# Optimization experiments

Hardware: AMD Instinct MI355X
Metric: run time of the kernel (lower is better)

Reference implementation:

```python
import math
import jax, jax.numpy as jnp
import numpy as np

GROUPS = 32
EPS = 1e-5


def group_norm(x, w, b):
    # x: [B, C, H, W]
    B, C, H, W = x.shape
    xg = x.reshape(B, GROUPS, C // GROUPS, H, W)
    mean = xg.mean(axis=(2, 3, 4), keepdims=True)
    var = xg.var(axis=(2, 3, 4), keepdims=True)
    xg = (xg - mean) * jax.lax.rsqrt(var + EPS)
    x = xg.reshape(B, C, H, W)
    return x * w[None, :, None, None] + b[None, :, None, None]


def setup_inputs() -> dict:
    key = jax.random.key(0)
    ks = jax.random.split(key, 4)
    B, C, H, W = 16, 512, 32, 32
    x = jax.random.normal(ks[0], (B, C, H, W), dtype=jnp.float32)
    norm_w = jnp.ones((C,), dtype=jnp.float32)
    norm_b = jnp.zeros((C,), dtype=jnp.float32)
    qkv_w = jax.random.normal(ks[1], (3 * C, C), dtype=jnp.float32) / math.sqrt(C)
    qkv_b = jnp.zeros((3 * C,), dtype=jnp.float32)
    proj_w = jax.random.normal(ks[2], (C, C), dtype=jnp.float32) / math.sqrt(C)
    proj_b = jnp.zeros((C,), dtype=jnp.float32)
    return {"x": x, "norm_w": norm_w, "norm_b": norm_b,
            "qkv_w": qkv_w, "qkv_b": qkv_b,
            "proj_w": proj_w, "proj_b": proj_b}


def reference(x, norm_w, norm_b, qkv_w, qkv_b, proj_w, proj_b):
    B, C, H, W = x.shape
    xn = group_norm(x, norm_w, norm_b)
    # 1x1 conv == channel matmul: [B,3C,H,W]
    qkv = jnp.einsum('oc,bchw->bohw', qkv_w, xn) + qkv_b[None, :, None, None]
    q, k, v = jnp.split(qkv, 3, axis=1)
    q = q.reshape(B, C, H * W).transpose(0, 2, 1)  # [B, HW, C]
    k = k.reshape(B, C, H * W)                     # [B, C, HW]
    v = v.reshape(B, C, H * W).transpose(0, 2, 1)  # [B, HW, C]
    attn = jax.nn.softmax(jnp.einsum('bnc,bcm->bnm', q, k) / math.sqrt(C), axis=-1)
    h = jnp.einsum('bnm,bmc->bnc', attn, v)        # [B, HW, C]
    h = h.transpose(0, 2, 1).reshape(B, C, H, W)
    out = jnp.einsum('oc,bchw->bohw', proj_w, h) + proj_b[None, :, None, None]
    return out + x
```

## Files before the change

### kernel.cpp

```cpp
#include <hip/hip_runtime.h>

#define GLD16(gp, lp) __builtin_amdgcn_global_load_lds( \
    (const __attribute__((address_space(1))) void*)(gp), \
    (__attribute__((address_space(3))) void*)(lp), 16, 0, 0)

typedef __attribute__((ext_vector_type(8))) short bf16x8;
typedef __attribute__((ext_vector_type(4))) float f32x4;

__device__ __forceinline__ short f2bf(float f) {
    union { float f; unsigned u; } x; x.f = f;
    unsigned r = x.u + 0x7fffu + ((x.u >> 16) & 1u);
    return (short)(r >> 16);
}
__device__ __forceinline__ float bf2f(short s) {
    union { unsigned u; float f; } x;
    x.u = ((unsigned)(unsigned short)s) << 16;
    return x.f;
}
__device__ __forceinline__ int xcd_swz(int id, int n) {
    return (id & 7) * (n >> 3) + (id >> 3);
}

__global__ __launch_bounds__(256) void prep(
    const float* __restrict__ qkv_w, const float* __restrict__ proj_w,
    short* __restrict__ wq, short* __restrict__ wp,
    const float* __restrict__ x, float* __restrict__ mean, float* __restrict__ rstd)
{
    if (blockIdx.x < 1024) {
        int idx = blockIdx.x * 256 + threadIdx.x;
        const int NQ4 = (1536 * 512) / 4;
        float4 f; short4 s;
        if (idx < NQ4) {
            f = ((const float4*)qkv_w)[idx];
            s.x = f2bf(f.x); s.y = f2bf(f.y); s.z = f2bf(f.z); s.w = f2bf(f.w);
            ((short4*)wq)[idx] = s;
        } else {
            int j = idx - NQ4;
            f = ((const float4*)proj_w)[j];
            s.x = f2bf(f.x); s.y = f2bf(f.y); s.z = f2bf(f.z); s.w = f2bf(f.w);
            ((short4*)wp)[j] = s;
        }
    } else {
        int bg = blockIdx.x - 1024;
        const float4* p = (const float4*)(x + (size_t)bg * 16384);
        float s = 0.f, ss = 0.f;
        for (int i = threadIdx.x; i < 4096; i += 256) {
            float4 v = p[i];
            s  += v.x + v.y + v.z + v.w;
            ss += v.x * v.x + v.y * v.y + v.z * v.z + v.w * v.w;
        }
        #pragma unroll
        for (int o = 32; o > 0; o >>= 1) {
            s  += __shfl_down(s, o);
            ss += __shfl_down(ss, o);
        }
        __shared__ float ls[4], lss[4];
        int wave = threadIdx.x >> 6;
        if ((threadIdx.x & 63) == 0) { ls[wave] = s; lss[wave] = ss; }
        __syncthreads();
        if (threadIdx.x == 0) {
            s  = ls[0] + ls[1] + ls[2] + ls[3];
            ss = lss[0] + lss[1] + lss[2] + lss[3];
            float m = s * (1.f / 16384.f);
            float var = ss * (1.f / 16384.f) - m * m;
            mean[bg] = m;
            rstd[bg] = rsqrtf(var + 1e-5f);
        }
    }
}

__global__ __launch_bounds__(256) void gn_apply_t(
    const float* __restrict__ x, const float* __restrict__ w, const float* __restrict__ bb,
    const float* __restrict__ mean, const float* __restrict__ rstd,
    short* __restrict__ xnT)
{
    __shared__ short tile[64][65];
    int b = blockIdx.z, cblk = blockIdx.y, nblk = blockIdx.x;
    int t = threadIdx.x;
    int nl = t & 63;
    int cb = t >> 6;
    #pragma unroll
    for (int i = 0; i < 16; ++i) {
        int cl = cb * 16 + i;
        int cg = cblk * 64 + cl;
        int bgid = b * 32 + (cg >> 4);
        float sc = rstd[bgid] * w[cg];
        float sh = bb[cg] - mean[bgid] * sc;
        float xv = x[((size_t)(b * 512 + cg)) * 1024 + nblk * 64 + nl];
        tile[cl][nl] = f2bf(xv * sc + sh);
    }
    __syncthreads();
    int ng = t >> 4;
    int c4 = (t & 15) * 4;
    #pragma unroll
    for (int p = 0; p < 4; ++p) {
        int nl2 = p * 16 + ng;
        short4 sv;
        sv.x = tile[c4 + 0][nl2];
        sv.y = tile[c4 + 1][nl2];
        sv.z = tile[c4 + 2][nl2];
        sv.w = tile[c4 + 3][nl2];
        *(short4*)&xnT[((size_t)(b * 1024 + nblk * 64 + nl2)) * 512 + cblk * 64 + c4] = sv;
    }
}

template<int NT>
__device__ __forceinline__ void gemm256_8p(
    const short* __restrict__ A, const short* __restrict__ B,
    const int lda, const int ldb, short* lds, f32x4 acc[8][4])
{
    const int tid  = threadIdx.x;
    const int lane = tid & 63;
    const int wave = tid >> 6;
    const int wm = wave >> 2;
    const int wn = wave & 3;
    const int fr = lane & 15;
    const int fk = lane >> 4;

    const short* pa[2]; const short* pb[2]; int la[2], lb[2];
    #pragma unroll
    for (int i = 0; i < 2; ++i) {
        int cid = i * 512 + tid;
        int row = cid >> 2, sl = cid & 3;
        int csw = sl ^ ((row >> 1) & 3);
        pa[i] = A + (size_t)row * lda + csw * 8;
        pb[i] = B + (size_t)row * ldb + csw * 8;
        la[i] = cid * 8;
        lb[i] = 8192 + cid * 8;
    }

    #pragma unroll
    for (int i = 0; i < 2; ++i) GLD16(pa[i],      lds + la[i]);
    #pragma unroll
    for (int i = 0; i < 2; ++i) GLD16(pb[i],      lds + lb[i]);
    #pragma unroll
    for (int i = 0; i < 2; ++i) GLD16(pa[i] + 32, lds + 16384 + la[i]);
    #pragma unroll
    for (int i = 0; i < 2; ++i) GLD16(pb[i] + 32, lds + 16384 + lb[i]);
    asm volatile("s_waitcnt vmcnt(4)" ::: "memory");
    asm volatile("s_barrier" ::: "memory");

    const int arow0 = wm * 128 + fr;
    const int brow0 = wn * 64 + fr;

    int base = 0, sbase = 32768, kst = 64;
    for (int t = 0; t < NT; ++t) {
        const short* lA = lds + base;
        const short* lB = lds + base + 8192;
        const bool pre = (t + 2 < NT);

        if (pre) {
            GLD16(pa[0] + kst, lds + sbase + la[0]);
            GLD16(pa[1] + kst, lds + sbase + la[1]);
        }
        bf16x8 af[8], bf0[2];
        #pragma unroll
        for (int m = 0; m < 8; ++m) {
            int R = arow0 + m * 16;
            af[m] = *(const bf16x8*)&lA[R * 32 + ((fk ^ ((R >> 1) & 3)) << 3)];
        }
        #pragma unroll
        for (int n = 0; n < 2; ++n) {
            int R = brow0 + n * 16;
            bf0[n] = *(const bf16x8*)&lB[R * 32 + ((fk ^ ((R >> 1) & 3)) << 3)];
        }
        asm volatile("s_barrier" ::: "memory");
        __builtin_amdgcn_s_setprio(1);
        #pragma unroll
        for (int m = 0; m < 8; ++m)
            #pragma unroll
            for (int n = 0; n < 2; ++n)
                acc[m][n] = __builtin_amdgcn_mfma_f32_16x16x32_bf16(af[m], bf0[n], acc[m][n], 0, 0, 0);
        __builtin_amdgcn_s_setprio(0);

        if (pre) {
            GLD16(pb[0] + kst, lds + sbase + lb[0]);
            GLD16(pb[1] + kst, lds + sbase + lb[1]);
        }
        bf16x8 bf1[2];
        #pragma unroll
        for (int n = 0; n < 2; ++n) {
            int R = brow0 + (n + 2) * 16;
            bf1[n] = *(const bf16x8*)&lB[R * 32 + ((fk ^ ((R >> 1) & 3)) << 3)];
        }
        asm volatile("s_barrier" ::: "memory");
        __builtin_amdgcn_s_setprio(1);
        #pragma unroll
        for (int m = 0; m < 8; ++m)
            #pragma unroll
            for (int n = 0; n < 2; ++n)
                acc[m][n + 2] = __builtin_amdgcn_mfma_f32_16x16x32_bf16(af[m], bf1[n], acc[m][n + 2], 0, 0, 0);
        __builtin_amdgcn_s_setprio(0);

        if (pre)                 asm volatile("s_waitcnt vmcnt(4)" ::: "memory");
        else if (t + 1 < NT)     asm volatile("s_waitcnt vmcnt(0)" ::: "memory");
        asm volatile("s_barrier" ::: "memory");
        __builtin_amdgcn_sched_barrier(0);
        base  = (base  == 32768) ? 0 : base  + 16384;
        sbase = (sbase == 32768) ? 0 : sbase + 16384;
        kst += 32;
    }
}

#define EPI_IDX() \
    const int lane = threadIdx.x & 63; \
    const int wave = threadIdx.x >> 6; \
    const int wm = wave >> 2; \
    const int wn = wave & 3; \
    const int fq = lane >> 4; \
    const int fcol = lane & 15;

__global__ __launch_bounds__(512, 2) void qkv_gemm(
    const short* __restrict__ wq, const float* __restrict__ qkv_b,
    const short* __restrict__ xnT,
    short* __restrict__ qT, short* __restrict__ kT, short* __restrict__ vv)
{
    __shared__ short lds[49152];
    int wg = xcd_swz(blockIdx.x, 384);
    const int bn = wg & 3, bm = (wg >> 2) % 6, b = wg / 24;
    const short* A  = wq + (size_t)bm * 256 * 512;
    const short* Bb = xnT + ((size_t)b * 1024 + bn * 256) * 512;
    f32x4 acc[8][4];
    #pragma unroll
    for (int m = 0; m < 8; ++m)
        #pragma unroll
        for (int n = 0; n < 4; ++n) acc[m][n] = (f32x4){0.f, 0.f, 0.f, 0.f};
    gemm256_8p<16>(A, Bb, 512, 512, lds, acc);

    EPI_IDX();
    const int region = bm >> 1;
    const float qscale = 0.04419417382415922f;

    #pragma unroll
    for (int m = 0; m < 8; ++m) {
        int o0 = bm * 256 + wm * 128 + m * 16 + fq * 4;
        float4 bias = *(const float4*)&qkv_b[o0];
        float bb4[4] = {bias.x, bias.y, bias.z, bias.w};
        #pragma unroll
        for (int n = 0; n < 4; ++n) {
            int col = bn * 256 + wn * 64 + n * 16 + fcol;
            f32x4 a = acc[m][n];
            if (region == 0) {
                short4 sv;
                sv.x = f2bf((a[0] + bb4[0]) * qscale);
                sv.y = f2bf((a[1] + bb4[1]) * qscale);
                sv.z = f2bf((a[2] + bb4[2]) * qscale);
                sv.w = f2bf((a[3] + bb4[3]) * qscale);
                *(short4*)&qT[((size_t)(b * 1024 + col)) * 512 + o0] = sv;
            } else if (region == 1) {
                short4 sv;
                sv.x = f2bf(a[0] + bb4[0]);
                sv.y = f2bf(a[1] + bb4[1]);
                sv.z = f2bf(a[2] + bb4[2]);
                sv.w = f2bf(a[3] + bb4[3]);
                *(short4*)&kT[((size_t)(b * 1024 + col)) * 512 + (o0 - 512)] = sv;
            } else {
                #pragma unroll
                for (int r = 0; r < 4; ++r)
                    vv[((size_t)(b * 512 + (o0 - 1024 + r))) * 1024 + col] = f2bf(a[r] + bb4[r]);
            }
        }
    }
}

__global__ __launch_bounds__(512, 2) void s_gemm(
    const short* __restrict__ kT, const short* __restrict__ qT, short* __restrict__ S)
{
    __shared__ short lds[49152];
    int wg = xcd_swz(blockIdx.x, 256);
    const int bn = wg & 3, bm = (wg >> 2) & 3, b = wg >> 4;
    const short* A  = kT + ((size_t)b * 1024 + bm * 256) * 512;
    const short* Bb = qT + ((size_t)b * 1024 + bn * 256) * 512;
    f32x4 acc[8][4];
    #pragma unroll
    for (int m = 0; m < 8; ++m)
        #pragma unroll
        for (int n = 0; n < 4; ++n) acc[m][n] = (f32x4){0.f, 0.f, 0.f, 0.f};
    gemm256_8p<16>(A, Bb, 512, 512, lds, acc);

    EPI_IDX();
    #pragma unroll
    for (int m = 0; m < 8; ++m) {
        int m0 = bm * 256 + wm * 128 + m * 16 + fq * 4;
        #pragma unroll
        for (int n = 0; n < 4; ++n) {
            int ncol = bn * 256 + wn * 64 + n * 16 + fcol;
            f32x4 a = acc[m][n];
            short4 sv;
            sv.x = f2bf(a[0]); sv.y = f2bf(a[1]); sv.z = f2bf(a[2]); sv.w = f2bf(a[3]);
            *(short4*)&S[((size_t)(b * 1024 + ncol)) * 1024 + m0] = sv;
        }
    }
}

__global__ __launch_bounds__(256) void softmax_rows(short* __restrict__ S)
{
    const int wave = threadIdx.x >> 6;
    const int lane = threadIdx.x & 63;
    size_t row = (size_t)blockIdx.x * 4 + wave;
    short* p = S + row * 1024;
    short4 raw[4];
    float v[16];
    #pragma unroll
    for (int i = 0; i < 4; ++i) raw[i] = ((short4*)p)[lane + 64 * i];
    #pragma unroll
    for (int i = 0; i < 4; ++i) {
        v[i * 4 + 0] = bf2f(raw[i].x);
        v[i * 4 + 1] = bf2f(raw[i].y);
        v[i * 4 + 2] = bf2f(raw[i].z);
        v[i * 4 + 3] = bf2f(raw[i].w);
    }
    float mx = v[0];
    #pragma unroll
    for (int i = 1; i < 16; ++i) mx = fmaxf(mx, v[i]);
    #pragma unroll
    for (int o = 1; o < 64; o <<= 1) mx = fmaxf(mx, __shfl_xor(mx, o));
    float sum = 0.f;
    #pragma unroll
    for (int i = 0; i < 16; ++i) { v[i] = __expf(v[i] - mx); sum += v[i]; }
    #pragma unroll
    for (int o = 1; o < 64; o <<= 1) sum += __shfl_xor(sum, o);
    float inv = 1.f / sum;
    #pragma unroll
    for (int i = 0; i < 4; ++i) {
        short4 sv;
        sv.x = f2bf(v[i * 4 + 0] * inv);
        sv.y = f2bf(v[i * 4 + 1] * inv);
        sv.z = f2bf(v[i * 4 + 2] * inv);
        sv.w = f2bf(v[i * 4 + 3] * inv);
        ((short4*)p)[lane + 64 * i] = sv;
    }
}

__global__ __launch_bounds__(512, 2) void pv_gemm(
    const short* __restrict__ vv, const short* __restrict__ P, short* __restrict__ h)
{
    __shared__ short lds[49152];
    int wg = xcd_swz(blockIdx.x, 128);
    const int bn = wg & 3, bm = (wg >> 2) & 1, b = wg >> 3;
    const short* A  = vv + ((size_t)b * 512 + bm * 256) * 1024;
    const short* Bb = P + ((size_t)b * 1024 + bn * 256) * 1024;
    f32x4 acc[8][4];
    #pragma unroll
    for (int m = 0; m < 8; ++m)
        #pragma unroll
        for (int n = 0; n < 4; ++n) acc[m][n] = (f32x4){0.f, 0.f, 0.f, 0.f};
    gemm256_8p<32>(A, Bb, 1024, 1024, lds, acc);

    EPI_IDX();
    #pragma unroll
    for (int m = 0; m < 8; ++m) {
        int c0 = bm * 256 + wm * 128 + m * 16 + fq * 4;
        #pragma unroll
        for (int n = 0; n < 4; ++n) {
            int ncol = bn * 256 + wn * 64 + n * 16 + fcol;
            f32x4 a = acc[m][n];
            short4 sv;
            sv.x = f2bf(a[0]); sv.y = f2bf(a[1]); sv.z = f2bf(a[2]); sv.w = f2bf(a[3]);
            *(short4*)&h[((size_t)(b * 1024 + ncol)) * 512 + c0] = sv;
        }
    }
}

__global__ __launch_bounds__(512, 2) void proj_gemm(
    const short* __restrict__ wp, const float* __restrict__ proj_b,
    const short* __restrict__ h, const float* __restrict__ x, float* __restrict__ out)
{
    __shared__ short lds[49152];
    int wg = xcd_swz(blockIdx.x, 128);
    const int bn = wg & 3, bm = (wg >> 2) & 1, b = wg >> 3;
    const short* A  = wp + (size_t)bm * 256 * 512;
    const short* Bb = h + ((size_t)b * 1024 + bn * 256) * 512;
    f32x4 acc[8][4];
    #pragma unroll
    for (int m = 0; m < 8; ++m)
        #pragma unroll
        for (int n = 0; n < 4; ++n) acc[m][n] = (f32x4){0.f, 0.f, 0.f, 0.f};
    gemm256_8p<16>(A, Bb, 512, 512, lds, acc);

    EPI_IDX();
    #pragma unroll
    for (int m = 0; m < 8; ++m) {
        int o0 = bm * 256 + wm * 128 + m * 16 + fq * 4;
        float4 pb = *(const float4*)&proj_b[o0];
        float pb4[4] = {pb.x, pb.y, pb.z, pb.w};
        #pragma unroll
        for (int n = 0; n < 4; ++n) {
            int col = bn * 256 + wn * 64 + n * 16 + fcol;
            f32x4 a = acc[m][n];
            #pragma unroll
            for (int r = 0; r < 4; ++r) {
                size_t idx = ((size_t)(b * 512 + o0 + r)) * 1024 + col;
                out[idx] = a[r] + pb4[r] + x[idx];
            }
        }
    }
}

extern "C" void kernel_launch(void* const* d_in, const int* in_sizes, int n_in,
                              void* d_out, int out_size, void* d_ws, size_t ws_size,
                              hipStream_t stream) {
    const float* x      = (const float*)d_in[0];
    const float* norm_w = (const float*)d_in[1];
    const float* norm_b = (const float*)d_in[2];
    const float* qkv_w  = (const float*)d_in[3];
    const float* qkv_b  = (const float*)d_in[4];
    const float* proj_w = (const float*)d_in[5];
    const float* proj_b = (const float*)d_in[6];
    float* out = (float*)d_out;

    char* ws = (char*)d_ws;
    size_t off = 0;
    auto alloc = [&](size_t bytes) {
        void* p = ws + off;
        off = (off + bytes + 255) & ~(size_t)255;
        return p;
    };
    float* mean = (float*)alloc(512 * 4);
    float* rstd = (float*)alloc(512 * 4);
    short* wq   = (short*)alloc((size_t)1536 * 512 * 2);
    short* wp   = (short*)alloc((size_t)512 * 512 * 2);
    short* xnT  = (short*)alloc((size_t)16 * 1024 * 512 * 2);
    short* qT   = (short*)alloc((size_t)16 * 1024 * 512 * 2);
    short* kT   = (short*)alloc((size_t)16 * 1024 * 512 * 2);
    short* vv   = (short*)alloc((size_t)16 * 512 * 1024 * 2);
    short* S    = (short*)alloc((size_t)16 * 1024 * 1024 * 2);
    short* h    = xnT;

    prep<<<1536, 256, 0, stream>>>(qkv_w, proj_w, wq, wp, x, mean, rstd);
    gn_apply_t<<<dim3(16, 8, 16), 256, 0, stream>>>(x, norm_w, norm_b, mean, rstd, xnT);
    qkv_gemm<<<384, 512, 0, stream>>>(wq, qkv_b, xnT, qT, kT, vv);
    s_gemm<<<256, 512, 0, stream>>>(kT, qT, S);
    softmax_rows<<<4096, 256, 0, stream>>>(S);
    pv_gemm<<<128, 512, 0, stream>>>(vv, S, h);
    proj_gemm<<<128, 512, 0, stream>>>(wp, proj_b, h, x, out);
}
```

Measured before the change: 243.1 us.

## Use 128x256 GEMM tiles for PV and projection to double workgroup count

Adds a 128x256 tile GEMM variant with a smaller 3-stage LDS footprint and uses it for pv_gemm and proj_gemm, so each launches 256 workgroups instead of 128. The goal is to fill more of the 256 CUs, which were underused by the two smaller GEMMs. It also remaps the qkv and proj tile indices to treat batch and spatial as one flattened N dimension. Smaller tiles lower per-block data reuse and raise global traffic for the A operand.

```diff
diff --git a/kernel.cpp b/kernel.cpp
--- a/kernel.cpp
+++ b/kernel.cpp
@@ -202,7 +202,105 @@
     }
 }
 
-#define EPI_IDX() \
+template<int NT>
+__device__ __forceinline__ void gemm128x256(
+    const short* __restrict__ A, const short* __restrict__ B,
+    const int lda, const int ldb, short* lds, f32x4 acc[4][4])
+{
+    const int tid  = threadIdx.x;
+    const int lane = tid & 63;
+    const int wave = tid >> 6;
+    const int wm = wave >> 2;
+    const int wn = wave & 3;
+    const int fr = lane & 15;
+    const int fk = lane >> 4;
+
+    const short* pa; int la;
+    {
+        int row = tid >> 2, sl = tid & 3;
+        int csw = sl ^ ((row >> 1) & 3);
+        pa = A + (size_t)row * lda + csw * 8;
+        la = tid * 8;
+    }
+    const short* pb[2]; int lb[2];
+    #pragma unroll
+    for (int i = 0; i < 2; ++i) {
+        int cid = i * 512 + tid;
+        int row = cid >> 2, sl = cid & 3;
+        int csw = sl ^ ((row >> 1) & 3);
+        pb[i] = B + (size_t)row * ldb + csw * 8;
+        lb[i] = 4096 + cid * 8;
+    }
+
+    GLD16(pa, lds + la);
+    #pragma unroll
+    for (int i = 0; i < 2; ++i) GLD16(pb[i], lds + lb[i]);
+    GLD16(pa + 32, lds + 12288 + la);
+    #pragma unroll
+    for (int i = 0; i < 2; ++i) GLD16(pb[i] + 32, lds + 12288 + lb[i]);
+    asm volatile("s_waitcnt vmcnt(3)" ::: "memory");
+    asm volatile("s_barrier" ::: "memory");
+
+    const int arow0 = wm * 64 + fr;
+    const int brow0 = wn * 64 + fr;
+
+    int base = 0, sbase = 24576, kst = 64;
+    for (int t = 0; t < NT; ++t) {
+        const short* lA = lds + base;
+        const short* lB = lds + base + 4096;
+        const bool pre = (t + 2 < NT);
+
+        if (pre) GLD16(pa + kst, lds + sbase + la);
+        bf16x8 af[4], bf0[2];
+        #pragma unroll
+        for (int m = 0; m < 4; ++m) {
+            int R = arow0 + m * 16;
+            af[m] = *(const bf16x8*)&lA[R * 32 + ((fk ^ ((R >> 1) & 3)) << 3)];
+        }
+        #pragma unroll
+        for (int n = 0; n < 2; ++n) {
+            int R = brow0 + n * 16;
+            bf0[n] = *(const bf16x8*)&lB[R * 32 + ((fk ^ ((R >> 1) & 3)) << 3)];
+        }
+        asm volatile("s_barrier" ::: "memory");
+        __builtin_amdgcn_s_setprio(1);
+        #pragma unroll
+        for (int m = 0; m < 4; ++m)
+            #pragma unroll
+            for (int n = 0; n < 2; ++n)
+                acc[m][n] = __builtin_amdgcn_mfma_f32_16x16x32_bf16(af[m], bf0[n], acc[m][n], 0, 0, 0);
+        __builtin_amdgcn_s_setprio(0);
+
+        if (pre) {
+            GLD16(pb[0] + kst, lds + sbase + lb[0]);
+            GLD16(pb[1] + kst, lds + sbase + lb[1]);
+        }
+        bf16x8 bf1[2];
+        #pragma unroll
+        for (int n = 0; n < 2; ++n) {
+            int R = brow0 + (n + 2) * 16;
+            bf1[n] = *(const bf16x8*)&lB[R * 32 + ((fk ^ ((R >> 1) & 3)) << 3)];
+        }
+        asm volatile("s_barrier" ::: "memory");
+        __builtin_amdgcn_s_setprio(1);
+        #pragma unroll
+        for (int m = 0; m < 4; ++m)
+            #pragma unroll
+            for (int n = 0; n < 2; ++n)
+                acc[m][n + 2] = __builtin_amdgcn_mfma_f32_16x16x32_bf16(af[m], bf1[n], acc[m][n + 2], 0, 0, 0);
+        __builtin_amdgcn_s_setprio(0);
+
+        if (pre)                 asm volatile("s_waitcnt vmcnt(3)" ::: "memory");
+        else if (t + 1 < NT)     asm volatile("s_waitcnt vmcnt(0)" ::: "memory");
+        asm volatile("s_barrier" ::: "memory");
+        __builtin_amdgcn_sched_barrier(0);
+        base  = (base  == 24576) ? 0 : base  + 12288;
+        sbase = (sbase == 24576) ? 0 : sbase + 12288;
+        kst += 32;
+    }
+}
+
+#define EPI_IDX8() \
     const int lane = threadIdx.x & 63; \
     const int wave = threadIdx.x >> 6; \
     const int wm = wave >> 2; \
@@ -217,9 +315,9 @@
 {
     __shared__ short lds[49152];
     int wg = xcd_swz(blockIdx.x, 384);
-    const int bn = wg & 3, bm = (wg >> 2) % 6, b = wg / 24;
+    const int bm = wg % 6, bn = wg / 6;
     const short* A  = wq + (size_t)bm * 256 * 512;
-    const short* Bb = xnT + ((size_t)b * 1024 + bn * 256) * 512;
+    const short* Bb = xnT + (size_t)bn * 256 * 512;
     f32x4 acc[8][4];
     #pragma unroll
     for (int m = 0; m < 8; ++m)
@@ -227,7 +325,7 @@
         for (int n = 0; n < 4; ++n) acc[m][n] = (f32x4){0.f, 0.f, 0.f, 0.f};
     gemm256_8p<16>(A, Bb, 512, 512, lds, acc);
 
-    EPI_IDX();
+    EPI_IDX8();
     const int region = bm >> 1;
     const float qscale = 0.04419417382415922f;
 
@@ -238,7 +336,8 @@
         float bb4[4] = {bias.x, bias.y, bias.z, bias.w};
         #pragma unroll
         for (int n = 0; n < 4; ++n) {
-            int col = bn * 256 + wn * 64 + n * 16 + fcol;
+            int cf = bn * 256 + wn * 64 + n * 16 + fcol;
+            int b = cf >> 10, col = cf & 1023;
             f32x4 a = acc[m][n];
             if (region == 0) {
                 short4 sv;
@@ -278,7 +377,7 @@
         for (int n = 0; n < 4; ++n) acc[m][n] = (f32x4){0.f, 0.f, 0.f, 0.f};
     gemm256_8p<16>(A, Bb, 512, 512, lds, acc);
 
-    EPI_IDX();
+    EPI_IDX8();
     #pragma unroll
     for (int m = 0; m < 8; ++m) {
         int m0 = bm * 256 + wm * 128 + m * 16 + fq * 4;
@@ -332,25 +431,25 @@
     }
 }
 
-__global__ __launch_bounds__(512, 2) void pv_gemm(
+__global__ __launch_bounds__(512, 4) void pv_gemm(
     const short* __restrict__ vv, const short* __restrict__ P, short* __restrict__ h)
 {
-    __shared__ short lds[49152];
-    int wg = xcd_swz(blockIdx.x, 128);
-    const int bn = wg & 3, bm = (wg >> 2) & 1, b = wg >> 3;
-    const short* A  = vv + ((size_t)b * 512 + bm * 256) * 1024;
+    __shared__ short lds[36864];
+    int wg = xcd_swz(blockIdx.x, 256);
+    const int bn = wg & 3, bm = (wg >> 2) & 3, b = wg >> 4;
+    const short* A  = vv + ((size_t)b * 512 + bm * 128) * 1024;
     const short* Bb = P + ((size_t)b * 1024 + bn * 256) * 1024;
-    f32x4 acc[8][4];
-    #pragma unroll
-    for (int m = 0; m < 8; ++m)
+    f32x4 acc[4][4];
+    #pragma unroll
+    for (int m = 0; m < 4; ++m)
         #pragma unroll
         for (int n = 0; n < 4; ++n) acc[m][n] = (f32x4){0.f, 0.f, 0.f, 0.f};
-    gemm256_8p<32>(A, Bb, 1024, 1024, lds, acc);
-
-    EPI_IDX();
-    #pragma unroll
-    for (int m = 0; m < 8; ++m) {
-        int c0 = bm * 256 + wm * 128 + m * 16 + fq * 4;
+    gemm128x256<32>(A, Bb, 1024, 1024, lds, acc);
+
+    EPI_IDX8();
+    #pragma unroll
+    for (int m = 0; m < 4; ++m) {
+        int c0 = bm * 128 + wm * 64 + m * 16 + fq * 4;
         #pragma unroll
         for (int n = 0; n < 4; ++n) {
             int ncol = bn * 256 + wn * 64 + n * 16 + fcol;
@@ -362,31 +461,32 @@
     }
 }
 
-__global__ __launch_bounds__(512, 2) void proj_gemm(
+__global__ __launch_bounds__(512, 4) void proj_gemm(
     const short* __restrict__ wp, const float* __restrict__ proj_b,
     const short* __restrict__ h, const float* __restrict__ x, float* __restrict__ out)
 {
-    __shared__ short lds[49152];
-    int wg = xcd_swz(blockIdx.x, 128);
-    const int bn = wg & 3, bm = (wg >> 2) & 1, b = wg >> 3;
-    const short* A  = wp + (size_t)bm * 256 * 512;
-    const short* Bb = h + ((size_t)b * 1024 + bn * 256) * 512;
-    f32x4 acc[8][4];
-    #pragma unroll
-    for (int m = 0; m < 8; ++m)
+    __shared__ short lds[36864];
+    int wg = xcd_swz(blockIdx.x, 256);
+    const int bm = wg & 3, bn = wg >> 2;
+    const short* A  = wp + (size_t)bm * 128 * 512;
+    const short* Bb = h + (size_t)bn * 256 * 512;
+    f32x4 acc[4][4];
+    #pragma unroll
+    for (int m = 0; m < 4; ++m)
         #pragma unroll
         for (int n = 0; n < 4; ++n) acc[m][n] = (f32x4){0.f, 0.f, 0.f, 0.f};
-    gemm256_8p<16>(A, Bb, 512, 512, lds, acc);
-
-    EPI_IDX();
-    #pragma unroll
-    for (int m = 0; m < 8; ++m) {
-        int o0 = bm * 256 + wm * 128 + m * 16 + fq * 4;
+    gemm128x256<16>(A, Bb, 512, 512, lds, acc);
+
+    EPI_IDX8();
+    #pragma unroll
+    for (int m = 0; m < 4; ++m) {
+        int o0 = bm * 128 + wm * 64 + m * 16 + fq * 4;
         float4 pb = *(const float4*)&proj_b[o0];
         float pb4[4] = {pb.x, pb.y, pb.z, pb.w};
         #pragma unroll
         for (int n = 0; n < 4; ++n) {
-            int col = bn * 256 + wn * 64 + n * 16 + fcol;
+            int cf = bn * 256 + wn * 64 + n * 16 + fcol;
+            int b = cf >> 10, col = cf & 1023;
             f32x4 a = acc[m][n];
             #pragma unroll
             for (int r = 0; r < 4; ++r) {
@@ -432,6 +532,6 @@
     qkv_gemm<<<384, 512, 0, stream>>>(wq, qkv_b, xnT, qT, kT, vv);
     s_gemm<<<256, 512, 0, stream>>>(kT, qT, S);
     softmax_rows<<<4096, 256, 0, stream>>>(S);
-    pv_gemm<<<128, 512, 0, stream>>>(vv, S, h);
-    proj_gemm<<<128, 512, 0, stream>>>(wp, proj_b, h, x, out);
-}
+    pv_gemm<<<256, 512, 0, stream>>>(vv, S, h);
+    proj_gemm<<<256, 512, 0, stream>>>(wp, proj_b, h, x, out);
+}
```

New measurement: 228.3 us. 1.06x faster.
